# Performance work log

Hardware: AMD Instinct MI355X
Metric: run time of the kernel (lower is better)

The kernel has to match this reference:

```python
import jax, jax.numpy as jnp
import numpy as np

NEG = -1e9
BN_EPS = 1e-3  # keras BatchNormalization default epsilon
LRELU = 0.2    # GAT leaky-relu slope


def _gat(Xt, bias_mat, Wg, a1, a2, bg):
    """Dense multi-head GAT (Velickovic TF impl).
    Xt: [B,N,F], bias_mat: [B,N,N] additive mask (0 / -1e9).
    Wg: [H,F,D], a1/a2/bg: [H,D]. Returns [B,N,H*D]."""
    feats = jnp.einsum('bnf,hfd->bhnd', Xt, Wg)          # [B,H,N,D]
    f1 = jnp.einsum('bhnd,hd->bhn', feats, a1)
    f2 = jnp.einsum('bhnd,hd->bhn', feats, a2)
    logits = f1[:, :, :, None] + f2[:, :, None, :]        # [B,H,N,N]
    logits = jax.nn.leaky_relu(logits, LRELU) + bias_mat[:, None]
    coefs = jax.nn.softmax(logits, axis=-1)
    vals = jnp.einsum('bhnm,bhmd->bhnd', coefs, feats) + bg[None, :, None, :]
    vals = jax.nn.elu(vals)
    B, H, N, D = vals.shape
    return jnp.transpose(vals, (0, 2, 1, 3)).reshape(B, N, H * D)


def setup_inputs() -> dict:
    key = jax.random.key(0)
    ks = jax.random.split(key, 16)
    B, T, N, F = 4, 12, 2048, 64
    H, D = 4, 16           # attn_heads, hid_units
    C = H * D              # out_channels = 64

    X = jax.random.normal(ks[0], (B, T, N, F), dtype=jnp.float32)
    # random sparse adjacency (~avg degree 16) + self loops -> additive mask
    adj = jax.random.uniform(ks[1], (B, N, N)) < (16.0 / N)
    adj = adj | jnp.eye(N, dtype=bool)[None]
    bias_mat = jnp.where(adj, 0.0, NEG).astype(jnp.float32)

    he = lambda k, s: jax.random.normal(k, s, dtype=jnp.float32) * np.sqrt(2.0 / s[-2] if len(s) > 1 else 2.0 / s[-1])
    return {
        'X': X, 'bias_mat': bias_mat,
        'W_z': he(ks[2], (F, C)), 'Z_bias': he(ks[3], (1, C)),
        'W_h': he(ks[4], (F, C)), 'H_bias': he(ks[5], (1, C)),
        'Wg_z': he(ks[6], (H, F, D)), 'a1_z': he(ks[7], (H, D)),
        'a2_z': he(ks[8], (H, D)), 'bg_z': jnp.zeros((H, D), jnp.float32),
        'Wg_h': he(ks[9], (H, F, D)), 'a1_h': he(ks[10], (H, D)),
        'a2_h': he(ks[11], (H, D)), 'bg_h': jnp.zeros((H, D), jnp.float32),
        'bn_gamma': jnp.ones((C,), jnp.float32), 'bn_beta': jnp.zeros((C,), jnp.float32),
        'bn_mean': jnp.zeros((C,), jnp.float32), 'bn_var': jnp.ones((C,), jnp.float32),
    }


def reference(X, bias_mat, W_z, Z_bias, W_h, H_bias,
              Wg_z, a1_z, a2_z, bg_z, Wg_h, a1_h, a2_h, bg_h,
              bn_gamma, bn_beta, bn_mean, bn_var):
    B, T, N, F = X.shape
    C = W_z.shape[1]
    H0 = jnp.zeros((B, N, C), dtype=jnp.float32)

    def step(Hc, Xt):
        Z = _gat(Xt, bias_mat, Wg_z, a1_z, a2_z, bg_z) + Xt @ W_z + Z_bias + Hc
        Z = jax.nn.sigmoid(Z)
        Tt = _gat(Xt, bias_mat, Wg_h, a1_h, a2_h, bg_h) + Hc + Xt @ W_h + H_bias
        Tt = jnp.tanh(Tt)
        Hn = Z * Hc + (1.0 - Z) * Tt
        return Hn, None

    Xs = jnp.transpose(X, (1, 0, 2, 3))  # [T,B,N,F]
    Hf, _ = jax.lax.scan(step, H0, Xs)
    # last_layer=True path: BatchNorm (inference, moving stats) on final H
    out = (Hf - bn_mean) * jax.lax.rsqrt(bn_var + BN_EPS) * bn_gamma + bn_beta
    return out
```

## Files before the change

### kernel.cpp

```cpp
#include <hip/hip_runtime.h>
#include <cstdint>
#include <cstddef>

#define NB 4
#define NT 12
#define NN 2048
#define NF 64
#define NH 4
#define ND 16
#define NC 64
#define MAXD 64
#define NR (NB * NT * NN)

typedef _Float16 f16x8 __attribute__((ext_vector_type(8)));
typedef _Float16 f16x2 __attribute__((ext_vector_type(2)));
typedef float f32x4 __attribute__((ext_vector_type(4)));

#define LR(v) ((v) >= 0.f ? (v) : 0.2f * (v))

__global__ __launch_bounds__(256) void build_adj_k(const float* __restrict__ bias,
                                                   int* __restrict__ adj,
                                                   int* __restrict__ deg) {
  int gtid = blockIdx.x * 256 + threadIdx.x;
  int wid = gtid >> 6;
  int lane = threadIdx.x & 63;
  if (wid >= NB * NN) return;
  const float* row = bias + (size_t)wid * NN;
  int* arow = adj + (size_t)wid * MAXD;
  int count = 0;
  for (int c0 = 0; c0 < NN; c0 += 64) {
    float v = __builtin_nontemporal_load(row + c0 + lane);
    bool e = (v > -1e8f);
    unsigned long long m = __ballot(e);
    int pre = __popcll(m & ((1ull << lane) - 1ull));
    if (e) {
      int pos = count + pre;
      if (pos < MAXD) arow[pos] = c0 + lane;
    }
    count += __popcll(m);
  }
  if (lane == 0) deg[wid] = count < MAXD ? count : MAXD;
}

__global__ __launch_bounds__(256) void mfma_gemm_k(
    const float* __restrict__ X,
    const float* __restrict__ Wgz, const float* __restrict__ Wgh,
    const float* __restrict__ Wz,  const float* __restrict__ Wh,
    const float* __restrict__ Zb,  const float* __restrict__ Hb,
    const float* __restrict__ a1z, const float* __restrict__ a2z,
    const float* __restrict__ a1h, const float* __restrict__ a2h,
    uint32_t* __restrict__ gbufF, float* __restrict__ gbufS,
    float* __restrict__ fbuf) {
  __shared__ _Float16 Ws16[272 * 72];
  __shared__ _Float16 Xs16[64 * 72];
  __shared__ float biasL[128];
  const int tid = threadIdx.x;
  const size_t row0 = (size_t)blockIdx.x * 64;

  for (int idx = tid; idx < 64 * 256; idx += 256) {
    int k = idx >> 8, c = idx & 255;
    float w;
    if (c < 64)       w = Wgz[((c >> 4) << 10) + (k << 4) + (c & 15)];
    else if (c < 128) { int ch = c - 64; w = Wgh[((ch >> 4) << 10) + (k << 4) + (ch & 15)]; }
    else              { int cl = c - 128; w = ((cl & 1) ? Wh : Wz)[(k << 6) + (cl >> 1)]; }
    Ws16[c * 72 + k] = (_Float16)w;
  }
  for (int idx = tid; idx < 16 * 64; idx += 256) {
    int j = idx >> 6, k = idx & 63, h = j & 3;
    const float* Wg = (j & 4) ? Wgh : Wgz;
    const float* av = (j & 8) ? ((j & 4) ? a2h : a2z) : ((j & 4) ? a1h : a1z);
    float s = 0.f;
#pragma unroll
    for (int d = 0; d < 16; d++)
      s = fmaf(Wg[(h << 10) + (k << 4) + d], av[(h << 4) + d], s);
    Ws16[(256 + j) * 72 + k] = (_Float16)s;
  }
  {
    const float4* Xg = (const float4*)(X + row0 * NF);
    for (int idx = tid; idx < 64 * 16; idx += 256) {
      int r = idx >> 4, k4 = idx & 15;
      float4 xv = Xg[idx];
      _Float16* d = &Xs16[r * 72 + k4 * 4];
      d[0] = (_Float16)xv.x; d[1] = (_Float16)xv.y;
      d[2] = (_Float16)xv.z; d[3] = (_Float16)xv.w;
    }
  }
  if (tid < 128) biasL[tid] = ((tid & 1) ? Hb : Zb)[tid >> 1];
  __syncthreads();

  const int wv = tid >> 6, lane = tid & 63;
  const int m = lane & 15, quad = lane >> 4;
  const int r0 = wv * 16;
  f16x8 A0 = *(const f16x8*)&Xs16[(r0 + m) * 72 + quad * 8];
  f16x8 A1 = *(const f16x8*)&Xs16[(r0 + m) * 72 + 32 + quad * 8];

  f32x4 zacc[4];
#pragma unroll
  for (int ct = 0; ct < 17; ct++) {
    const int c = ct * 16 + m;
    f16x8 B0 = *(const f16x8*)&Ws16[c * 72 + quad * 8];
    f16x8 B1 = *(const f16x8*)&Ws16[c * 72 + 32 + quad * 8];
    f32x4 acc = {0.f, 0.f, 0.f, 0.f};
    acc = __builtin_amdgcn_mfma_f32_16x16x32_f16(A0, B0, acc, 0, 0, 0);
    acc = __builtin_amdgcn_mfma_f32_16x16x32_f16(A1, B1, acc, 0, 0, 0);
    if (ct < 4) {
      zacc[ct] = acc;
    } else if (ct < 8) {
      const int ch = (ct - 4) * 16 + m;
#pragma unroll
      for (int r = 0; r < 4; r++) {
        f16x2 pv = {(_Float16)zacc[ct - 4][r], (_Float16)acc[r]};
        gbufF[(row0 + r0 + quad * 4 + r) * 64 + ch] =
            __builtin_bit_cast(uint32_t, pv);
      }
    } else if (ct < 16) {
      const int cs = (ct - 8) * 16 + m;
      const float bias = biasL[cs];
#pragma unroll
      for (int r = 0; r < 4; r++)
        gbufS[(row0 + r0 + quad * 4 + r) * 128 + cs] = acc[r] + bias;
    } else {
#pragma unroll
      for (int r = 0; r < 4; r++)
        fbuf[(row0 + r0 + quad * 4 + r) * 16 + m] = acc[r];
    }
  }
}

__global__ __launch_bounds__(256) void recur_all_k(
    const uint32_t* __restrict__ gbufF, const float* __restrict__ gbufS,
    const float* __restrict__ fbuf,
    const int* __restrict__ adj, const int* __restrict__ deg,
    const float* __restrict__ bgz, const float* __restrict__ bgh,
    const float* __restrict__ gam, const float* __restrict__ bet,
    const float* __restrict__ mu, const float* __restrict__ var,
    float* __restrict__ out) {
  __shared__ int   adjL[4][MAXD];
  __shared__ float wexp[4][8][68];
  const int lane = threadIdx.x & 63;
  const int ws = threadIdx.x >> 6;
  int bb = blockIdx.x;
  int node = (((bb & 7) << 8) + (bb >> 3)) * 4 + ws;
  const int b = node >> 11;
  const int nl = node & (NN - 1);
  const int dg = deg[node];
  adjL[ws][lane] = (lane < dg) ? adj[(size_t)node * MAXD + lane] : 0;
  const int dgp = (dg + 7) & ~7;

  const int ch = lane, hh = lane >> 4;
  const float bz = bgz[ch], bh = bgh[ch];
  float hc = 0.f;

#pragma unroll 1
  for (int t = 0; t < NT; t++) {
    const size_t rbase = ((size_t)b * NT + t) * NN;
    const float* fb = fbuf + rbase * 16;
    const uint32_t* gF = gbufF + rbase * 64;
    const float* gS = gbufS + rbase * 128;

    {
      const float4* p = (const float4*)(fb + (size_t)nl * 16);
      int mm = adjL[ws][lane];
      const float4* q = (const float4*)(fb + (size_t)mm * 16);
      float4 f1z = p[0], f1h = p[1], f2z = q[2], f2h = q[3];
      bool act = lane < dg;
      wexp[ws][0][lane] = act ? __expf(LR(f1z.x + f2z.x)) : 0.f;
      wexp[ws][1][lane] = act ? __expf(LR(f1z.y + f2z.y)) : 0.f;
      wexp[ws][2][lane] = act ? __expf(LR(f1z.z + f2z.z)) : 0.f;
      wexp[ws][3][lane] = act ? __expf(LR(f1z.w + f2z.w)) : 0.f;
      wexp[ws][4][lane] = act ? __expf(LR(f1h.x + f2h.x)) : 0.f;
      wexp[ws][5][lane] = act ? __expf(LR(f1h.y + f2h.y)) : 0.f;
      wexp[ws][6][lane] = act ? __expf(LR(f1h.z + f2h.z)) : 0.f;
      wexp[ws][7][lane] = act ? __expf(LR(f1h.w + f2h.w)) : 0.f;
    }

    float az = 0.f, ah = 0.f, sz = 0.f, sh = 0.f;
    const float* wz = wexp[ws][hh];
    const float* wh = wexp[ws][4 + hh];
    for (int mi = 0; mi < dgp; mi += 8) {
      int4 ma = *(const int4*)&adjL[ws][mi];
      int4 mb = *(const int4*)&adjL[ws][mi + 4];
      float4 wza = *(const float4*)&wz[mi];
      float4 wzb = *(const float4*)&wz[mi + 4];
      float4 wha = *(const float4*)&wh[mi];
      float4 whb = *(const float4*)&wh[mi + 4];
      uint32_t d0 = gF[(size_t)ma.x * 64 + ch];
      uint32_t d1 = gF[(size_t)ma.y * 64 + ch];
      uint32_t d2 = gF[(size_t)ma.z * 64 + ch];
      uint32_t d3 = gF[(size_t)ma.w * 64 + ch];
      uint32_t d4 = gF[(size_t)mb.x * 64 + ch];
      uint32_t d5 = gF[(size_t)mb.y * 64 + ch];
      uint32_t d6 = gF[(size_t)mb.z * 64 + ch];
      uint32_t d7 = gF[(size_t)mb.w * 64 + ch];
      f16x2 p0 = __builtin_bit_cast(f16x2, d0);
      f16x2 p1 = __builtin_bit_cast(f16x2, d1);
      f16x2 p2 = __builtin_bit_cast(f16x2, d2);
      f16x2 p3 = __builtin_bit_cast(f16x2, d3);
      f16x2 p4 = __builtin_bit_cast(f16x2, d4);
      f16x2 p5 = __builtin_bit_cast(f16x2, d5);
      f16x2 p6 = __builtin_bit_cast(f16x2, d6);
      f16x2 p7 = __builtin_bit_cast(f16x2, d7);
      az = fmaf(wza.x, (float)p0.x, az); ah = fmaf(wha.x, (float)p0.y, ah);
      az = fmaf(wza.y, (float)p1.x, az); ah = fmaf(wha.y, (float)p1.y, ah);
      az = fmaf(wza.z, (float)p2.x, az); ah = fmaf(wha.z, (float)p2.y, ah);
      az = fmaf(wza.w, (float)p3.x, az); ah = fmaf(wha.w, (float)p3.y, ah);
      az = fmaf(wzb.x, (float)p4.x, az); ah = fmaf(whb.x, (float)p4.y, ah);
      az = fmaf(wzb.y, (float)p5.x, az); ah = fmaf(whb.y, (float)p5.y, ah);
      az = fmaf(wzb.z, (float)p6.x, az); ah = fmaf(whb.z, (float)p6.y, ah);
      az = fmaf(wzb.w, (float)p7.x, az); ah = fmaf(whb.w, (float)p7.y, ah);
      sz += (wza.x + wza.y) + (wza.z + wza.w) + (wzb.x + wzb.y) + (wzb.z + wzb.w);
      sh += (wha.x + wha.y) + (wha.z + wha.w) + (whb.x + whb.y) + (whb.z + whb.w);
    }
    az /= sz;
    ah /= sh;

    float2 sp = *(const float2*)(gS + (size_t)nl * 128 + 2 * ch);
    float vz = az + bz; vz = vz > 0.f ? vz : expm1f(vz);
    float zg = 1.f / (1.f + __expf(-(vz + sp.x + hc)));
    float vh = ah + bh; vh = vh > 0.f ? vh : expm1f(vh);
    float tg = tanhf(vh + sp.y + hc);
    hc = zg * hc + (1.f - zg) * tg;
  }
  out[(size_t)node * 64 + ch] =
      (hc - mu[ch]) * rsqrtf(var[ch] + 1e-3f) * gam[ch] + bet[ch];
}

extern "C" void kernel_launch(void* const* d_in, const int* in_sizes, int n_in,
                              void* d_out, int out_size, void* d_ws, size_t ws_size,
                              hipStream_t stream) {
  (void)in_sizes; (void)n_in; (void)out_size; (void)ws_size;
  const float* X   = (const float*)d_in[0];
  const float* bm  = (const float*)d_in[1];
  const float* Wz  = (const float*)d_in[2];
  const float* Zb  = (const float*)d_in[3];
  const float* Wh  = (const float*)d_in[4];
  const float* Hb  = (const float*)d_in[5];
  const float* Wgz = (const float*)d_in[6];
  const float* a1z = (const float*)d_in[7];
  const float* a2z = (const float*)d_in[8];
  const float* bgz = (const float*)d_in[9];
  const float* Wgh = (const float*)d_in[10];
  const float* a1h = (const float*)d_in[11];
  const float* a2h = (const float*)d_in[12];
  const float* bgh = (const float*)d_in[13];
  const float* gam = (const float*)d_in[14];
  const float* bet = (const float*)d_in[15];
  const float* mu  = (const float*)d_in[16];
  const float* var = (const float*)d_in[17];
  float* out = (float*)d_out;

  char* p = (char*)d_ws;
  uint32_t* gbufF = (uint32_t*)p; p += (size_t)NR * 64 * sizeof(uint32_t);
  float*    gbufS = (float*)p;    p += (size_t)NR * 128 * sizeof(float);
  float*    fbuf  = (float*)p;    p += (size_t)NR * 16 * sizeof(float);
  int*      adj   = (int*)p;      p += (size_t)NB * NN * MAXD * sizeof(int);
  int*      deg   = (int*)p;      p += (size_t)NB * NN * sizeof(int);

  build_adj_k<<<dim3(NB * NN / 4), dim3(256), 0, stream>>>(bm, adj, deg);
  mfma_gemm_k<<<dim3(NR / 64), dim3(256), 0, stream>>>(
      X, Wgz, Wgh, Wz, Wh, Zb, Hb, a1z, a2z, a1h, a2h, gbufF, gbufS, fbuf);
  recur_all_k<<<dim3(NB * NN / 4), dim3(256), 0, stream>>>(
      gbufF, gbufS, fbuf, adj, deg, bgz, bgh, gam, bet, mu, var, out);
}
```

Before: 265.2 us.

## Precompute fp16 weights once, pack skip terms as fp16, use fast math intrinsics

Adds a small prep kernel that builds the fp16 combined weight matrix and bias vector once, instead of every GEMM block rebuilding them in shared memory. The GEMM block now loads X directly into registers. The X@W skip terms are stored as packed fp16 pairs rather than fp32, which halves that buffer's traffic. The recurrence replaces divisions, expm1f and tanhf with rcp/exp approximations and uses 32-bit index arithmetic. In exchange, precision drops in the skip terms and activations, and there is one extra kernel launch.

```diff
diff --git a/kernel.cpp b/kernel.cpp
--- a/kernel.cpp
+++ b/kernel.cpp
@@ -17,6 +17,7 @@
 typedef float f32x4 __attribute__((ext_vector_type(4)));
 
 #define LR(v) ((v) >= 0.f ? (v) : 0.2f * (v))
+#define RCPF(x) __builtin_amdgcn_rcpf(x)
 
 __global__ __launch_bounds__(256) void build_adj_k(const float* __restrict__ bias,
                                                    int* __restrict__ adj,
@@ -42,93 +43,103 @@
   if (lane == 0) deg[wid] = count < MAXD ? count : MAXD;
 }
 
-__global__ __launch_bounds__(256) void mfma_gemm_k(
-    const float* __restrict__ X,
+__global__ __launch_bounds__(256) void prep_w_k(
     const float* __restrict__ Wgz, const float* __restrict__ Wgh,
     const float* __restrict__ Wz,  const float* __restrict__ Wh,
-    const float* __restrict__ Zb,  const float* __restrict__ Hb,
     const float* __restrict__ a1z, const float* __restrict__ a2z,
     const float* __restrict__ a1h, const float* __restrict__ a2h,
-    uint32_t* __restrict__ gbufF, float* __restrict__ gbufS,
-    float* __restrict__ fbuf) {
-  __shared__ _Float16 Ws16[272 * 72];
-  __shared__ _Float16 Xs16[64 * 72];
-  __shared__ float biasL[128];
-  const int tid = threadIdx.x;
-  const size_t row0 = (size_t)blockIdx.x * 64;
-
-  for (int idx = tid; idx < 64 * 256; idx += 256) {
-    int k = idx >> 8, c = idx & 255;
+    const float* __restrict__ Zb,  const float* __restrict__ Hb,
+    _Float16* __restrict__ W16, float* __restrict__ biasC) {
+  int idx = blockIdx.x * 256 + threadIdx.x;
+  if (idx < 272 * 64) {
+    int c = idx >> 6, k = idx & 63;
     float w;
     if (c < 64)       w = Wgz[((c >> 4) << 10) + (k << 4) + (c & 15)];
-    else if (c < 128) { int ch = c - 64; w = Wgh[((ch >> 4) << 10) + (k << 4) + (ch & 15)]; }
-    else              { int cl = c - 128; w = ((cl & 1) ? Wh : Wz)[(k << 6) + (cl >> 1)]; }
-    Ws16[c * 72 + k] = (_Float16)w;
-  }
-  for (int idx = tid; idx < 16 * 64; idx += 256) {
-    int j = idx >> 6, k = idx & 63, h = j & 3;
-    const float* Wg = (j & 4) ? Wgh : Wgz;
-    const float* av = (j & 8) ? ((j & 4) ? a2h : a2z) : ((j & 4) ? a1h : a1z);
-    float s = 0.f;
-#pragma unroll
-    for (int d = 0; d < 16; d++)
-      s = fmaf(Wg[(h << 10) + (k << 4) + d], av[(h << 4) + d], s);
-    Ws16[(256 + j) * 72 + k] = (_Float16)s;
-  }
-  {
-    const float4* Xg = (const float4*)(X + row0 * NF);
-    for (int idx = tid; idx < 64 * 16; idx += 256) {
-      int r = idx >> 4, k4 = idx & 15;
-      float4 xv = Xg[idx];
-      _Float16* d = &Xs16[r * 72 + k4 * 4];
-      d[0] = (_Float16)xv.x; d[1] = (_Float16)xv.y;
-      d[2] = (_Float16)xv.z; d[3] = (_Float16)xv.w;
-    }
-  }
-  if (tid < 128) biasL[tid] = ((tid & 1) ? Hb : Zb)[tid >> 1];
-  __syncthreads();
-
+    else if (c < 128) { int q = c - 64; w = Wgh[((q >> 4) << 10) + (k << 4) + (q & 15)]; }
+    else if (c < 192) w = Wz[(k << 6) + (c - 128)];
+    else if (c < 256) w = Wh[(k << 6) + (c - 192)];
+    else {
+      int j = c - 256, h = j & 3;
+      const float* Wg = (j & 4) ? Wgh : Wgz;
+      const float* av = (j & 8) ? ((j & 4) ? a2h : a2z) : ((j & 4) ? a1h : a1z);
+      float s = 0.f;
+#pragma unroll
+      for (int d = 0; d < 16; d++)
+        s = fmaf(Wg[(h << 10) + (k << 4) + d], av[(h << 4) + d], s);
+      w = s;
+    }
+    W16[idx] = (_Float16)w;
+  }
+  if (blockIdx.x == 0 && threadIdx.x < 128)
+    biasC[threadIdx.x] =
+        (threadIdx.x < 64) ? Zb[threadIdx.x] : Hb[threadIdx.x - 64];
+}
+
+__global__ __launch_bounds__(256) void mfma_gemm_k(
+    const float* __restrict__ X, const _Float16* __restrict__ W16,
+    const float* __restrict__ biasC,
+    uint32_t* __restrict__ gbufF, uint32_t* __restrict__ gbufS,
+    float* __restrict__ fbuf) {
+  const int tid = threadIdx.x;
   const int wv = tid >> 6, lane = tid & 63;
   const int m = lane & 15, quad = lane >> 4;
-  const int r0 = wv * 16;
-  f16x8 A0 = *(const f16x8*)&Xs16[(r0 + m) * 72 + quad * 8];
-  f16x8 A1 = *(const f16x8*)&Xs16[(r0 + m) * 72 + 32 + quad * 8];
-
-  f32x4 zacc[4];
+  const unsigned rw = blockIdx.x * 64 + wv * 16;
+
+  const float* xr = X + (size_t)(rw + m) * 64;
+  float4 x0 = *(const float4*)(xr + quad * 8);
+  float4 x1 = *(const float4*)(xr + quad * 8 + 4);
+  float4 x2 = *(const float4*)(xr + 32 + quad * 8);
+  float4 x3 = *(const float4*)(xr + 32 + quad * 8 + 4);
+  f16x8 A0 = {(_Float16)x0.x, (_Float16)x0.y, (_Float16)x0.z, (_Float16)x0.w,
+              (_Float16)x1.x, (_Float16)x1.y, (_Float16)x1.z, (_Float16)x1.w};
+  f16x8 A1 = {(_Float16)x2.x, (_Float16)x2.y, (_Float16)x2.z, (_Float16)x2.w,
+              (_Float16)x3.x, (_Float16)x3.y, (_Float16)x3.z, (_Float16)x3.w};
+
+  float bzc[4], bhc[4];
+#pragma unroll
+  for (int j = 0; j < 4; j++) {
+    bzc[j] = biasC[j * 16 + m];
+    bhc[j] = biasC[64 + j * 16 + m];
+  }
+
+  f32x4 zacc[4], zs[4];
 #pragma unroll
   for (int ct = 0; ct < 17; ct++) {
-    const int c = ct * 16 + m;
-    f16x8 B0 = *(const f16x8*)&Ws16[c * 72 + quad * 8];
-    f16x8 B1 = *(const f16x8*)&Ws16[c * 72 + 32 + quad * 8];
+    const _Float16* wp = W16 + (ct * 16 + m) * 64;
+    f16x8 B0 = *(const f16x8*)(wp + quad * 8);
+    f16x8 B1 = *(const f16x8*)(wp + 32 + quad * 8);
     f32x4 acc = {0.f, 0.f, 0.f, 0.f};
     acc = __builtin_amdgcn_mfma_f32_16x16x32_f16(A0, B0, acc, 0, 0, 0);
     acc = __builtin_amdgcn_mfma_f32_16x16x32_f16(A1, B1, acc, 0, 0, 0);
+    const unsigned rb = rw + quad * 4;
     if (ct < 4) {
       zacc[ct] = acc;
     } else if (ct < 8) {
-      const int ch = (ct - 4) * 16 + m;
+      const int chn = (ct - 4) * 16 + m;
 #pragma unroll
       for (int r = 0; r < 4; r++) {
         f16x2 pv = {(_Float16)zacc[ct - 4][r], (_Float16)acc[r]};
-        gbufF[(row0 + r0 + quad * 4 + r) * 64 + ch] =
-            __builtin_bit_cast(uint32_t, pv);
+        gbufF[(rb + r) * 64 + chn] = __builtin_bit_cast(uint32_t, pv);
       }
+    } else if (ct < 12) {
+#pragma unroll
+      for (int r = 0; r < 4; r++) zs[ct - 8][r] = acc[r] + bzc[ct - 8];
     } else if (ct < 16) {
-      const int cs = (ct - 8) * 16 + m;
-      const float bias = biasL[cs];
-#pragma unroll
-      for (int r = 0; r < 4; r++)
-        gbufS[(row0 + r0 + quad * 4 + r) * 128 + cs] = acc[r] + bias;
+      const int chn = (ct - 12) * 16 + m;
+#pragma unroll
+      for (int r = 0; r < 4; r++) {
+        f16x2 pv = {(_Float16)zs[ct - 12][r], (_Float16)(acc[r] + bhc[ct - 12])};
+        gbufS[(rb + r) * 64 + chn] = __builtin_bit_cast(uint32_t, pv);
+      }
     } else {
 #pragma unroll
-      for (int r = 0; r < 4; r++)
-        fbuf[(row0 + r0 + quad * 4 + r) * 16 + m] = acc[r];
+      for (int r = 0; r < 4; r++) fbuf[(size_t)(rb + r) * 16 + m] = acc[r];
     }
   }
 }
 
 __global__ __launch_bounds__(256) void recur_all_k(
-    const uint32_t* __restrict__ gbufF, const float* __restrict__ gbufS,
+    const uint32_t* __restrict__ gbufF, const uint32_t* __restrict__ gbufS,
     const float* __restrict__ fbuf,
     const int* __restrict__ adj, const int* __restrict__ deg,
     const float* __restrict__ bgz, const float* __restrict__ bgh,
@@ -144,7 +155,7 @@
   const int b = node >> 11;
   const int nl = node & (NN - 1);
   const int dg = deg[node];
-  adjL[ws][lane] = (lane < dg) ? adj[(size_t)node * MAXD + lane] : 0;
+  adjL[ws][lane] = (lane < dg) ? adj[node * MAXD + lane] : 0;
   const int dgp = (dg + 7) & ~7;
 
   const int ch = lane, hh = lane >> 4;
@@ -153,15 +164,15 @@
 
 #pragma unroll 1
   for (int t = 0; t < NT; t++) {
-    const size_t rbase = ((size_t)b * NT + t) * NN;
-    const float* fb = fbuf + rbase * 16;
-    const uint32_t* gF = gbufF + rbase * 64;
-    const float* gS = gbufS + rbase * 128;
+    const unsigned rb = (unsigned)(b * NT + t) * NN;
+    const float* fb = fbuf + (size_t)rb * 16;
+    const uint32_t* gF = gbufF + (size_t)rb * 64;
+    const uint32_t* gS = gbufS + (size_t)rb * 64;
 
     {
-      const float4* p = (const float4*)(fb + (size_t)nl * 16);
+      const float4* p = (const float4*)(fb + nl * 16);
       int mm = adjL[ws][lane];
-      const float4* q = (const float4*)(fb + (size_t)mm * 16);
+      const float4* q = (const float4*)(fb + mm * 16);
       float4 f1z = p[0], f1h = p[1], f2z = q[2], f2h = q[3];
       bool act = lane < dg;
       wexp[ws][0][lane] = act ? __expf(LR(f1z.x + f2z.x)) : 0.f;
@@ -184,14 +195,14 @@
       float4 wzb = *(const float4*)&wz[mi + 4];
       float4 wha = *(const float4*)&wh[mi];
       float4 whb = *(const float4*)&wh[mi + 4];
-      uint32_t d0 = gF[(size_t)ma.x * 64 + ch];
-      uint32_t d1 = gF[(size_t)ma.y * 64 + ch];
-      uint32_t d2 = gF[(size_t)ma.z * 64 + ch];
-      uint32_t d3 = gF[(size_t)ma.w * 64 + ch];
-      uint32_t d4 = gF[(size_t)mb.x * 64 + ch];
-      uint32_t d5 = gF[(size_t)mb.y * 64 + ch];
-      uint32_t d6 = gF[(size_t)mb.z * 64 + ch];
-      uint32_t d7 = gF[(size_t)mb.w * 64 + ch];
+      uint32_t d0 = gF[(ma.x << 6) + ch];
+      uint32_t d1 = gF[(ma.y << 6) + ch];
+      uint32_t d2 = gF[(ma.z << 6) + ch];
+      uint32_t d3 = gF[(ma.w << 6) + ch];
+      uint32_t d4 = gF[(mb.x << 6) + ch];
+      uint32_t d5 = gF[(mb.y << 6) + ch];
+      uint32_t d6 = gF[(mb.z << 6) + ch];
+      uint32_t d7 = gF[(mb.w << 6) + ch];
       f16x2 p0 = __builtin_bit_cast(f16x2, d0);
       f16x2 p1 = __builtin_bit_cast(f16x2, d1);
       f16x2 p2 = __builtin_bit_cast(f16x2, d2);
@@ -211,14 +222,16 @@
       sz += (wza.x + wza.y) + (wza.z + wza.w) + (wzb.x + wzb.y) + (wzb.z + wzb.w);
       sh += (wha.x + wha.y) + (wha.z + wha.w) + (whb.x + whb.y) + (whb.z + whb.w);
     }
-    az /= sz;
-    ah /= sh;
-
-    float2 sp = *(const float2*)(gS + (size_t)nl * 128 + 2 * ch);
-    float vz = az + bz; vz = vz > 0.f ? vz : expm1f(vz);
-    float zg = 1.f / (1.f + __expf(-(vz + sp.x + hc)));
-    float vh = ah + bh; vh = vh > 0.f ? vh : expm1f(vh);
-    float tg = tanhf(vh + sp.y + hc);
+    az *= RCPF(sz);
+    ah *= RCPF(sh);
+
+    f16x2 sp = __builtin_bit_cast(f16x2, gS[(nl << 6) + ch]);
+    float spx = (float)sp.x, spy = (float)sp.y;
+    float vz = az + bz; vz = vz > 0.f ? vz : __expf(vz) - 1.f;
+    float zg = RCPF(1.f + __expf(-(vz + spx + hc)));
+    float vh = ah + bh; vh = vh > 0.f ? vh : __expf(vh) - 1.f;
+    float ta = vh + spy + hc;
+    float tg = 1.f - 2.f * RCPF(__expf(2.f * ta) + 1.f);
     hc = zg * hc + (1.f - zg) * tg;
   }
   out[(size_t)node * 64 + ch] =
@@ -251,14 +264,18 @@
 
   char* p = (char*)d_ws;
   uint32_t* gbufF = (uint32_t*)p; p += (size_t)NR * 64 * sizeof(uint32_t);
-  float*    gbufS = (float*)p;    p += (size_t)NR * 128 * sizeof(float);
+  uint32_t* gbufS = (uint32_t*)p; p += (size_t)NR * 64 * sizeof(uint32_t);
   float*    fbuf  = (float*)p;    p += (size_t)NR * 16 * sizeof(float);
   int*      adj   = (int*)p;      p += (size_t)NB * NN * MAXD * sizeof(int);
   int*      deg   = (int*)p;      p += (size_t)NB * NN * sizeof(int);
-
+  _Float16* W16   = (_Float16*)p; p += 272 * 64 * sizeof(_Float16);
+  float*    biasC = (float*)p;    p += 128 * sizeof(float);
+
+  prep_w_k<<<dim3(68), dim3(256), 0, stream>>>(
+      Wgz, Wgh, Wz, Wh, a1z, a2z, a1h, a2h, Zb, Hb, W16, biasC);
   build_adj_k<<<dim3(NB * NN / 4), dim3(256), 0, stream>>>(bm, adj, deg);
   mfma_gemm_k<<<dim3(NR / 64), dim3(256), 0, stream>>>(
-      X, Wgz, Wgh, Wz, Wh, Zb, Hb, a1z, a2z, a1h, a2h, gbufF, gbufS, fbuf);
+      X, W16, biasC, gbufF, gbufS, fbuf);
   recur_all_k<<<dim3(NB * NN / 4), dim3(256), 0, stream>>>(
       gbufF, gbufS, fbuf, adj, deg, bgz, bgh, gam, bet, mu, var, out);
 }
```

New measurement: 264.5 us. About the same (-0.3%).
